# Optimization experiments

Hardware: AMD Instinct MI355X
Metric: run time of the kernel (lower is better)

The kernel has to match this reference:

```python
import jax, jax.numpy as jnp
import numpy as np

VOCAB, E, H, L, B, OUT = 50000, 300, 300, 75, 2048, 5

def setup_inputs() -> dict:
    key = jax.random.key(0)
    ks = jax.random.split(key, 12)
    s_e = 1.0 / np.sqrt(E)
    s_h = 1.0 / np.sqrt(H)
    return {
        "input_sequences": jax.random.randint(ks[0], (B, L), 0, VOCAB),
        "emb": jax.random.normal(ks[1], (VOCAB, E), jnp.float32) * 0.1,
        "W_ih": jax.random.normal(ks[2], (3 * H, E), jnp.float32) * s_e,
        "W_hh": jax.random.normal(ks[3], (3 * H, H), jnp.float32) * s_h,
        "b_ih": jax.random.normal(ks[4], (3 * H,), jnp.float32) * s_h,
        "b_hh": jax.random.normal(ks[5], (3 * H,), jnp.float32) * s_h,
        "wCo_w": jax.random.normal(ks[6], (3 * H,), jnp.float32) * (1.0 / np.sqrt(3 * H)),
        "wCo_b": jax.random.normal(ks[7], (1,), jnp.float32) * 0.02,
        "Wmy_w": jax.random.normal(ks[8], (L,), jnp.float32) * (1.0 / np.sqrt(L)),
        "Wmy_b": jax.random.normal(ks[9], (1,), jnp.float32) * 0.02,
        "logits_w": jax.random.normal(ks[10], (OUT, H), jnp.float32) * s_h,
        "logits_b": jax.random.normal(ks[11], (OUT,), jnp.float32) * 0.02,
    }

def _gru(x_tm, W_ih, W_hh, b_ih, b_hh):
    # x_tm: (L, B, E) time-major. PyTorch GRU cell math.
    gx_all = jnp.einsum("lbe,ge->lbg", x_tm, W_ih) + b_ih  # (L, B, 3H)
    h0 = jnp.zeros((x_tm.shape[1], W_hh.shape[1]), x_tm.dtype)
    def step(h, gx):
        gh = h @ W_hh.T + b_hh
        xr, xz, xn = jnp.split(gx, 3, axis=-1)
        hr, hz, hn = jnp.split(gh, 3, axis=-1)
        r = jax.nn.sigmoid(xr + hr)
        z = jax.nn.sigmoid(xz + hz)
        n = jnp.tanh(xn + r * hn)
        h_new = (1.0 - z) * n + z * h
        return h_new, h_new
    _, ys = jax.lax.scan(step, h0, gx_all)
    return ys  # (L, B, H)

def reference(input_sequences, emb, W_ih, W_hh, b_ih, b_hh,
              wCo_w, wCo_b, Wmy_w, Wmy_b, logits_w, logits_b):
    x = emb[input_sequences]                      # (B, L, E)
    out_tm = _gru(x.transpose(1, 0, 2), W_ih, W_hh, b_ih, b_hh)  # (L, B, H)
    h = out_tm.transpose(1, 0, 2)                 # (B, L, H)
    # co_attention: s_ij = wCo @ cat(h_i, h_j, h_i*h_j) + b
    # computed WITHOUT materializing the (B, L, L, 3H) tensor:
    wa, wb, wc = jnp.split(wCo_w, 3)
    a = h @ wa                                    # (B, L)
    b = h @ wb                                    # (B, L)
    c = jnp.einsum("bid,bjd->bij", h * wc, h)     # (B, L, L)
    s = a[:, :, None] + b[:, None, :] + c + wCo_b[0]
    # zero the diagonal (mask = ones - diag)
    s = s * (1.0 - jnp.eye(s.shape[1], dtype=s.dtype))
    # Wmy: Linear(75, 1) over the j axis
    sm = s @ Wmy_w + Wmy_b[0]                     # (B, L)
    attn = jax.nn.softmax(sm, axis=1)             # softmax over i
    pooled = jnp.einsum("bi,bih->bh", attn, h)    # (B, H)
    return pooled @ logits_w.T + logits_b         # (B, OUT)
```

## Files before the change

### kernel.cpp

```cpp
#include <hip/hip_runtime.h>
#include <stdint.h>


typedef float f32x4 __attribute__((ext_vector_type(4)));
typedef short bf16x8 __attribute__((ext_vector_type(8)));
typedef unsigned short u16;
typedef u16 u16x8 __attribute__((ext_vector_type(8)));
typedef u16 u16x4 __attribute__((ext_vector_type(4)));

#define DI __device__ __forceinline__

template <int N> struct IC { static constexpr int v = N; };

DI float bf2f(u16 v) {
    uint32_t u = ((uint32_t)v) << 16;
    float f;
    __builtin_memcpy(&f, &u, 4);
    return f;
}
DI u16 f2bf(float f) {
    uint32_t u;
    __builtin_memcpy(&u, &f, 4);
    uint32_t r = u + 0x7fffu + ((u >> 16) & 1u);
    return (u16)(r >> 16);
}
DI u16 cvt1(const void* p, int i, int f32m) {
    return f32m ? f2bf(((const float*)p)[i]) : ((const u16*)p)[i];
}

DI int hswz(int L, int kt) { return L ^ kt ^ (((L >> 4) & 3) << 1); }

DI u16x8 load_row8(const u16* __restrict__ base, int e0) {
    u16x4 z = {0, 0, 0, 0};
    u16x4 lo = (e0 < 300) ? *(const u16x4*)(base + e0) : z;
    u16x4 hi = (e0 + 4 < 300) ? *(const u16x4*)(base + e0 + 4) : z;
    u16x8 r;
    r[0] = lo[0]; r[1] = lo[1]; r[2] = lo[2]; r[3] = lo[3];
    r[4] = hi[0]; r[5] = hi[1]; r[6] = hi[2]; r[7] = hi[3];
    return r;
}
DI u16x8 load_row8_f32(const float* __restrict__ base, int e0) {
    f32x4 z = {0.f, 0.f, 0.f, 0.f};
    f32x4 lo = (e0 < 300) ? *(const f32x4*)(base + e0) : z;
    f32x4 hi = (e0 + 4 < 300) ? *(const f32x4*)(base + e0 + 4) : z;
    u16x8 r;
    r[0] = f2bf(lo[0]); r[1] = f2bf(lo[1]); r[2] = f2bf(lo[2]); r[3] = f2bf(lo[3]);
    r[4] = f2bf(hi[0]); r[5] = f2bf(hi[1]); r[6] = f2bf(hi[2]); r[7] = f2bf(hi[3]);
    return r;
}

__global__ __launch_bounds__(256) void detect_dtype(const u16* __restrict__ raw,
                                                    int* __restrict__ flag) {
    __shared__ int cnt;
    if (threadIdx.x == 0) cnt = 0;
    __syncthreads();
    int local = 0;
    for (int i = threadIdx.x; i < 4096; i += 256) {
        int e = (raw[i] >> 7) & 0xFF;
        if (e >= 140) local++;
    }
    atomicAdd(&cnt, local);
    __syncthreads();
    if (threadIdx.x == 0) flag[0] = (cnt > 256) ? 1 : 0;
}

__global__ __launch_bounds__(256) void conv_big(const void* __restrict__ in,
                                                u16* __restrict__ outp, int n,
                                                const int* __restrict__ flag) {
    const int f32m = flag[0];
    int i0 = (blockIdx.x * 256 + threadIdx.x) * 8;
#pragma unroll
    for (int k = 0; k < 8; k++) {
        int i = i0 + k;
        if (i < n) outp[i] = cvt1(in, i, f32m);
    }
}

__global__ __launch_bounds__(256) void conv_smalls(
    const void* bih_r, const void* bhh_r, const void* wCo_r, const void* wCob_r,
    const void* Wmy_r, const void* Wmyb_r, const void* lw_r, const void* lb_r,
    u16* __restrict__ smalls, const int* __restrict__ flag) {
    const int f32m = flag[0];
    int t = blockIdx.x * 256 + threadIdx.x;
    if (t < 900) smalls[t] = cvt1(bih_r, t, f32m);
    else if (t < 1800) smalls[1024 + t - 900] = cvt1(bhh_r, t - 900, f32m);
    else if (t < 2700) smalls[2048 + t - 1800] = cvt1(wCo_r, t - 1800, f32m);
    else if (t < 2775) smalls[3072 + t - 2700] = cvt1(Wmy_r, t - 2700, f32m);
    else if (t < 4275) smalls[3200 + t - 2775] = cvt1(lw_r, t - 2775, f32m);
    else if (t < 4280) smalls[4704 + t - 4275] = cvt1(lb_r, t - 4275, f32m);
    else if (t == 4280) smalls[4712] = cvt1(wCob_r, 0, f32m);
    else if (t == 4281) smalls[4713] = cvt1(Wmyb_r, 0, f32m);
}

__global__ __launch_bounds__(256) void prep_img(const u16* __restrict__ W,
                                                u16* __restrict__ img) {
    int t = blockIdx.x * 256 + threadIdx.x;
    if (t >= 60 * 10 * 64) return;
    int lane = t & 63;
    int kt = (t >> 6) % 10;
    int nt = t / 640;
    int g = nt * 16 + (lane & 15);
    int gate = g / 320, u = g - gate * 320;
    int e0 = kt * 32 + (lane >> 4) * 8;
    u16x8 v;
    if (u < 300) {
        v = load_row8(W + (size_t)(gate * 300 + u) * 300, e0);
    } else {
        u16x8 z = {0, 0, 0, 0, 0, 0, 0, 0};
        v = z;
    }
    *(u16x8*)&img[(size_t)t * 8] = v;
}

__global__ __launch_bounds__(256) void zero_hstate(float* __restrict__ hs) {
    int t = blockIdx.x * 256 + threadIdx.x;
    f32x4 z = {0.f, 0.f, 0.f, 0.f};
    ((f32x4*)hs)[t] = z;
}

__global__ __launch_bounds__(256, 2) void gemm1_kernel(
    const int* __restrict__ seq, const void* __restrict__ emb_raw,
    const u16* __restrict__ Wimg, const u16* __restrict__ bih,
    _Float16* __restrict__ gxn, int ck, int phase, int BC, int bshift,
    const int* __restrict__ flag) {
    __shared__ int ids[192];
    __shared__ __align__(16) u16 Aimg[12 * 64 * 8];
    __shared__ __align__(16) u16 Bbuf[12 * 64 * 8];

    const int tid = threadIdx.x;
    const int lane = tid & 63, wv = tid >> 6, q = lane >> 4, c = lane & 15;
    const int m0 = blockIdx.x * 192;
    const int nb = blockIdx.y;
    const int f32m = flag[0];
    const size_t PL = (size_t)15 * BC * 320;

    if (tid < 192) {
        int m = m0 + tid;
        int bc = m & (BC - 1);
        int tp = m >> bshift;
        ids[tid] = seq[(size_t)(phase * BC + bc) * 75 + ck * 15 + tp];
    }
    __syncthreads();

    f32x4 acc[3][12];
#pragma unroll
    for (int mt = 0; mt < 3; mt++)
#pragma unroll
        for (int nt = 0; nt < 12; nt++) {
            f32x4 z = {0.f, 0.f, 0.f, 0.f};
            acc[mt][nt] = z;
        }

    for (int kt = 0; kt < 10; kt++) {
#pragma unroll
        for (int s = 0; s < 3; s++) {
            int o = tid + s * 256;
            int qq = o / 192;
            int r = o - qq * 192;
            int e0 = kt * 32 + qq * 8;
            u16x8 v = f32m ? load_row8_f32((const float*)emb_raw + (size_t)ids[r] * 300, e0)
                           : load_row8((const u16*)emb_raw + (size_t)ids[r] * 300, e0);
            *(u16x8*)&Aimg[(((r >> 4) * 64) + ((r & 15) | (qq << 4))) * 8] = v;
        }
#pragma unroll
        for (int s = 0; s < 3; s++) {
            int ch = tid + s * 256;
            *(u16x8*)&Bbuf[ch * 8] =
                *(const u16x8*)&Wimg[(((size_t)(nb * 12 + (ch >> 6)) * 10 + kt) * 64 + (ch & 63)) * 8];
        }
        __syncthreads();

        bf16x8 a[3];
#pragma unroll
        for (int mt = 0; mt < 3; mt++) {
            u16x8 tmp = *(const u16x8*)&Aimg[(((wv * 3 + mt) * 64) + lane) * 8];
            a[mt] = __builtin_bit_cast(bf16x8, tmp);
        }
#pragma unroll
        for (int nt = 0; nt < 12; nt++) {
            u16x8 tb = *(const u16x8*)&Bbuf[(nt * 64 + lane) * 8];
            bf16x8 b = __builtin_bit_cast(bf16x8, tb);
#pragma unroll
            for (int mt = 0; mt < 3; mt++)
                acc[mt][nt] = __builtin_amdgcn_mfma_f32_16x16x32_bf16(a[mt], b, acc[mt][nt], 0, 0, 0);
        }
        __syncthreads();
    }

#pragma unroll
    for (int nt = 0; nt < 12; nt++) {
        int g = nb * 192 + nt * 16 + c;
        int gate = g / 320, u = g - gate * 320;
        float bias = (u < 300) ? bf2f(bih[gate * 300 + u]) : 0.f;
        _Float16* gp = gxn + (size_t)gate * PL;
#pragma unroll
        for (int mt = 0; mt < 3; mt++) {
            int mrow = m0 + (wv * 3 + mt) * 16 + q * 4;
#pragma unroll
            for (int reg = 0; reg < 4; reg++) {
                gp[(size_t)(mrow + reg) * 320 + u] = (_Float16)(acc[mt][nt][reg] + bias);
            }
        }
    }
}

__global__ __launch_bounds__(512, 1) void gru_chunk(
    const _Float16* __restrict__ gxn, const u16* __restrict__ Wimg,
    const u16* __restrict__ bhh_g, u16* __restrict__ h_all,
    float* __restrict__ hstate, int ck, int BC) {
    __shared__ __align__(16) u16 Hhi[10 * 64 * 8];
    __shared__ __align__(16) u16 Hlo[10 * 64 * 8];
    __shared__ __align__(16) u16 Wlds[61440];

    const int tid = threadIdx.x;
    const int lane = tid & 63, wv = tid >> 6, q = lane >> 4, c = lane & 15;
    const int b0 = blockIdx.x * 16;
    const int wbase = (wv < 4) ? wv * 9216 : 36864 + (wv - 4) * 6144;
    const size_t PL = (size_t)15 * BC * 320;

    float bhh[3][3];
    float hm[3][4];

    auto STAGE = [&](int kt, int buf, auto NTIC) {
        constexpr int NTI = NTIC.v;
        u16* dst = &Wlds[wbase + buf * (NTI * 3 * 512)];
#pragma unroll
        for (int Ti = 0; Ti < NTI; Ti++)
#pragma unroll
            for (int g = 0; g < 3; g++) {
                int nt = g * 20 + (wv + 8 * Ti);
                __builtin_amdgcn_global_load_lds(
                    (const unsigned int*)(Wimg + (size_t)(nt * 10 + kt) * 512 + lane * 8),
                    (unsigned int*)(dst + (Ti * 3 + g) * 512), 16, 0, 0);
            }
    };

    if (wv < 4) STAGE(0, 0, IC<3>{}); else STAGE(0, 0, IC<2>{});

    auto INIT = [&](auto NTIC) {
        constexpr int NTI = NTIC.v;
#pragma unroll
        for (int Ti = 0; Ti < NTI; Ti++) {
            int T = wv + 8 * Ti;
            int u = T * 16 + c;
#pragma unroll
            for (int g = 0; g < 3; g++)
                bhh[Ti][g] = (u < 300) ? bf2f(bhh_g[g * 300 + u]) : 0.f;
            int kti = T >> 1;
            int qp = ((T & 1) << 1) | (c >> 3);
            int j = c & 7;
#pragma unroll
            for (int reg = 0; reg < 4; reg++) {
                int m = q * 4 + reg;
                float h = hstate[(size_t)(b0 + m) * 320 + u];
                hm[Ti][reg] = h;
                int idx = (kti * 64 + ((q * 4 + reg) | (qp << 4))) * 8 + j;
                u16 hi = f2bf(h);
                Hhi[idx] = hi;
                Hlo[idx] = f2bf(h - bf2f(hi));
            }
        }
    };
    if (wv < 4) INIT(IC<3>{}); else INIT(IC<2>{});
    __syncthreads();

    for (int tt = 0; tt < 15; tt++) {
        auto PH1 = [&](auto NTIC) {
            constexpr int NTI = NTIC.v;
            constexpr int NT3 = NTI * 3;
            float gxr[NTI][4], gxz[NTI][4], gxnv[NTI][4];
#pragma unroll
            for (int Ti = 0; Ti < NTI; Ti++) {
                int u = (wv + 8 * Ti) * 16 + c;
#pragma unroll
                for (int reg = 0; reg < 4; reg++) {
                    int m = q * 4 + reg;
                    size_t idx = (size_t)((size_t)tt * BC + b0 + m) * 320 + u;
                    gxr[Ti][reg] = (float)gxn[idx];
                    gxz[Ti][reg] = (float)gxn[PL + idx];
                    gxnv[Ti][reg] = (float)gxn[2 * PL + idx];
                }
            }

            f32x4 acc[NTI][3];
#pragma unroll
            for (int Ti = 0; Ti < NTI; Ti++)
#pragma unroll
                for (int g = 0; g < 3; g++) {
                    f32x4 z = {0.f, 0.f, 0.f, 0.f};
                    acc[Ti][g] = z;
                }

#pragma unroll 2
            for (int kt = 0; kt < 10; kt++) {
                if (kt < 9) STAGE(kt + 1, (kt + 1) & 1, NTIC);
                else if (tt < 14) STAGE(0, 0, NTIC);
                if (kt == 9 && tt == 14) {
                    asm volatile("s_waitcnt vmcnt(0)" ::: "memory");
                } else if constexpr (NTI == 3) {
                    asm volatile("s_waitcnt vmcnt(9)" ::: "memory");
                } else {
                    asm volatile("s_waitcnt vmcnt(6)" ::: "memory");
                }

                u16x8 th = *(const u16x8*)&Hhi[(kt * 64 + lane) * 8];
                u16x8 tl = *(const u16x8*)&Hlo[(kt * 64 + lane) * 8];
                bf16x8 ahi = __builtin_bit_cast(bf16x8, th);
                bf16x8 alo = __builtin_bit_cast(bf16x8, tl);
                const u16* wb = &Wlds[wbase + (kt & 1) * (NT3 * 512)];
#pragma unroll
                for (int Ti = 0; Ti < NTI; Ti++)
#pragma unroll
                    for (int g = 0; g < 3; g++) {
                        u16x8 tb = *(const u16x8*)&wb[(Ti * 3 + g) * 512 + lane * 8];
                        bf16x8 b = __builtin_bit_cast(bf16x8, tb);
                        acc[Ti][g] = __builtin_amdgcn_mfma_f32_16x16x32_bf16(
                            ahi, b, acc[Ti][g], 0, 0, 0);
                        acc[Ti][g] = __builtin_amdgcn_mfma_f32_16x16x32_bf16(
                            alo, b, acc[Ti][g], 0, 0, 0);
                    }
            }

            const int tglob = ck * 15 + tt;
#pragma unroll
            for (int Ti = 0; Ti < NTI; Ti++) {
                int u = (wv + 8 * Ti) * 16 + c;
#pragma unroll
                for (int reg = 0; reg < 4; reg++) {
                    int m = q * 4 + reg;
                    float xr = gxr[Ti][reg];
                    float xz = gxz[Ti][reg];
                    float xn = gxnv[Ti][reg];
                    float hr = acc[Ti][0][reg] + bhh[Ti][0];
                    float hz = acc[Ti][1][reg] + bhh[Ti][1];
                    float hn = acc[Ti][2][reg] + bhh[Ti][2];
                    float r = 1.f / (1.f + __expf(-(xr + hr)));
                    float z = 1.f / (1.f + __expf(-(xz + hz)));
                    float ex = __expf(2.f * (xn + r * hn));
                    float n = 1.f - 2.f / (ex + 1.f);
                    float h = (1.f - z) * n + z * hm[Ti][reg];
                    hm[Ti][reg] = h;
                    h_all[((size_t)tglob * BC + (b0 + m)) * 320 + u] = f2bf(h);
                }
            }
        };
        if (wv < 4) PH1(IC<3>{}); else PH1(IC<2>{});
        __syncthreads();

        auto FRAG = [&](auto NTIC) {
            constexpr int NTI = NTIC.v;
#pragma unroll
            for (int Ti = 0; Ti < NTI; Ti++) {
                int T = wv + 8 * Ti;
                int kti = T >> 1;
                int qp = ((T & 1) << 1) | (c >> 3);
                int j = c & 7;
#pragma unroll
                for (int reg = 0; reg < 4; reg++) {
                    int idx = (kti * 64 + ((q * 4 + reg) | (qp << 4))) * 8 + j;
                    float h = hm[Ti][reg];
                    u16 hi = f2bf(h);
                    Hhi[idx] = hi;
                    Hlo[idx] = f2bf(h - bf2f(hi));
                }
            }
        };
        if (wv < 4) FRAG(IC<3>{}); else FRAG(IC<2>{});
        __syncthreads();
    }

    auto PERSIST = [&](auto NTIC) {
        constexpr int NTI = NTIC.v;
#pragma unroll
        for (int Ti = 0; Ti < NTI; Ti++) {
            int u = (wv + 8 * Ti) * 16 + c;
#pragma unroll
            for (int reg = 0; reg < 4; reg++) {
                int m = q * 4 + reg;
                hstate[(size_t)(b0 + m) * 320 + u] = hm[Ti][reg];
            }
        }
    };
    if (wv < 4) PERSIST(IC<3>{}); else PERSIST(IC<2>{});
}

__global__ __launch_bounds__(256) void coattn_kernel(
    const u16* __restrict__ h_all, const u16* __restrict__ smalls,
    void* __restrict__ outv, const int* __restrict__ flag, int phase, int BC) {
    __shared__ __align__(16) u16 himg[5 * 10 * 64 * 8];
    __shared__ float smacc[80], aArr[80], bArr[80], diagArr[80], attn[80], smv[80];
    __shared__ float scal[2];
    __shared__ float logitsAcc[5];

    const u16* wCo = smalls + 2048;
    const u16* Wmy = smalls + 3072;
    const u16* lw = smalls + 3200;
    const u16* lb = smalls + 4704;
    const int f32out = flag[0];

    const int b = blockIdx.x;
    const int tid = threadIdx.x;
    const int lane = tid & 63, wv = tid >> 6, q = lane >> 4, c = lane & 15;

    for (int o = tid; o < 3200; o += 256) {
        int i = o / 40;
        int oc = o - i * 40;
        int kt = oc >> 2, qq = oc & 3;
        int e0 = kt * 32 + qq * 8;
        u16x8 v = {0, 0, 0, 0, 0, 0, 0, 0};
        if (i < 75) v = *(const u16x8*)(h_all + ((size_t)i * BC + b) * 320 + e0);
        *(u16x8*)&himg[(((i >> 4) * 10 + kt) * 64 + hswz((i & 15) | (qq << 4), kt)) * 8] = v;
    }
    if (tid < 80) {
        smacc[tid] = 0.f; aArr[tid] = 0.f; bArr[tid] = 0.f;
        diagArr[tid] = 0.f; attn[tid] = 0.f;
    }
    if (tid < 5) logitsAcc[tid] = 0.f;
    __syncthreads();

    for (int pass = 0; pass < 2; pass++) {
        int nt = (pass == 0) ? wv : 4;
        int jj = nt * 16 + c;
        bf16x8 bfr[10];
#pragma unroll
        for (int kt = 0; kt < 10; kt++) {
            int e0 = kt * 32 + q * 8;
            u16x8 res = {0, 0, 0, 0, 0, 0, 0, 0};
            if (jj < 75) {
                u16x8 hv = *(const u16x8*)&himg[((nt * 10 + kt) * 64 + hswz(lane, kt)) * 8];
                u16x8 wcv = load_row8(wCo + 600, e0);
#pragma unroll
                for (int j = 0; j < 8; j++) res[j] = f2bf(bf2f(hv[j]) * bf2f(wcv[j]));
            } else if (jj == 75) {
                res = load_row8(wCo, e0);
            } else if (jj == 76) {
                res = load_row8(wCo + 300, e0);
            }
            bfr[kt] = __builtin_bit_cast(bf16x8, res);
        }
        float wmyj = (jj < 75) ? bf2f(Wmy[jj]) : 0.f;

        int nmt = (pass == 0) ? 5 : (wv == 0 ? 2 : 1);
        for (int mi = 0; mi < nmt; mi++) {
            int mt = (pass == 0) ? mi : (wv == 0 ? mi * 4 : wv);
            f32x4 acc = {0.f, 0.f, 0.f, 0.f};
#pragma unroll
            for (int kt = 0; kt < 10; kt++) {
                u16x8 ta = *(const u16x8*)&himg[((mt * 10 + kt) * 64 + hswz(lane, kt)) * 8];
                bf16x8 a = __builtin_bit_cast(bf16x8, ta);
                acc = __builtin_amdgcn_mfma_f32_16x16x32_bf16(a, bfr[kt], acc, 0, 0, 0);
            }
#pragma unroll
            for (int reg = 0; reg < 4; reg++) {
                int i = mt * 16 + q * 4 + reg;
                float v = acc[reg];
                float p = v * wmyj;
                p += __shfl_xor(p, 1);
                p += __shfl_xor(p, 2);
                p += __shfl_xor(p, 4);
                p += __shfl_xor(p, 8);
                if (c == 0 && i < 75) atomicAdd(&smacc[i], p);
                if (jj == i && i < 75) diagArr[i] = v;
                if (jj == 75) aArr[i] = v;
                if (jj == 76) bArr[i] = v;
            }
        }
    }
    __syncthreads();

    if (tid < 64) {
        float w1 = bf2f(Wmy[tid]);
        float w2 = (tid + 64 < 75) ? bf2f(Wmy[tid + 64]) : 0.f;
        float s1 = w1 + w2;
        float s2 = w1 * bArr[tid] + ((tid + 64 < 75) ? w2 * bArr[tid + 64] : 0.f);
#pragma unroll
        for (int m = 1; m < 64; m <<= 1) {
            s1 += __shfl_xor(s1, m);
            s2 += __shfl_xor(s2, m);
        }
        if (tid == 0) { scal[0] = s1; scal[1] = s2; }
    }
    __syncthreads();

    float cb = bf2f(smalls[4712]);
    float wmyb = bf2f(smalls[4713]);
    if (tid < 75) {
        float Wi = bf2f(Wmy[tid]);
        smv[tid] = smacc[tid] - diagArr[tid] * Wi + (aArr[tid] + cb) * (scal[0] - Wi) +
                   scal[1] - bArr[tid] * Wi + wmyb;
    }
    __syncthreads();

    if (tid < 64) {
        float v1 = smv[tid];
        float v2 = (tid + 64 < 75) ? smv[tid + 64] : -1e30f;
        float mx = fmaxf(v1, v2);
#pragma unroll
        for (int m = 1; m < 64; m <<= 1) mx = fmaxf(mx, __shfl_xor(mx, m));
        float e1 = __expf(v1 - mx);
        float e2 = (tid + 64 < 75) ? __expf(v2 - mx) : 0.f;
        float s = e1 + e2;
#pragma unroll
        for (int m = 1; m < 64; m <<= 1) s += __shfl_xor(s, m);
        attn[tid] = e1 / s;
        if (tid + 64 < 75) attn[tid + 64] = e2 / s;
    }
    __syncthreads();

    const int d1 = tid, d2 = tid + 256;
    float pd1 = 0.f, pd2 = 0.f;
    {
        const int kt1 = d1 >> 5, qq1 = (d1 >> 3) & 3, j1 = d1 & 7;
        const int kt2 = d2 >> 5, qq2 = (d2 >> 3) & 3, j2 = d2 & 7;
        for (int i = 0; i < 75; i++) {
            float a = attn[i];
            int ih = i >> 4, il = i & 15;
            pd1 += a * bf2f(himg[((ih * 10 + kt1) * 64 + hswz(il | (qq1 << 4), kt1)) * 8 + j1]);
            if (wv == 0)
                pd2 += a * bf2f(himg[((ih * 10 + kt2) * 64 + hswz(il | (qq2 << 4), kt2)) * 8 + j2]);
        }
    }
#pragma unroll
    for (int o = 0; o < 5; o++) {
        float part = (d1 < 300) ? pd1 * bf2f(lw[o * 300 + d1]) : 0.f;
        if (wv == 0 && d2 < 300) part += pd2 * bf2f(lw[o * 300 + d2]);
#pragma unroll
        for (int m = 1; m < 64; m <<= 1) part += __shfl_xor(part, m);
        if (lane == 0) atomicAdd(&logitsAcc[o], part);
    }
    __syncthreads();

    if (tid < 5) {
        float v = logitsAcc[tid] + bf2f(lb[tid]);
        size_t idx = (size_t)(phase * BC + b) * 5 + tid;
        if (f32out) ((float*)outv)[idx] = v;
        else ((u16*)outv)[idx] = f2bf(v);
    }
}

extern "C" void kernel_launch(void* const* d_in, const int* in_sizes, int n_in,
                              void* d_out, int out_size, void* d_ws, size_t ws_size,
                              hipStream_t stream) {
    const int* seq = (const int*)d_in[0];

    char* p = (char*)d_ws;
    int* flag = (int*)p;
    u16* smalls = (u16*)(p + 16);
    u16* WihImg = (u16*)(p + 9488);
    u16* WhhImg = (u16*)(p + 623888);
    u16* Wih_c = (u16*)(p + 1238288);
    u16* Whh_c = (u16*)(p + 1778288);
    const unsigned long long fixed_end = 2318288ull;

    auto req = [&](long long BC) -> unsigned long long {
        return fixed_end + (unsigned long long)BC * 87680ull + 1048576ull;
    };
    int BC = 256, bshift = 8;
    if (ws_size >= req(2048)) { BC = 2048; bshift = 11; }
    else if (ws_size >= req(1024)) { BC = 1024; bshift = 10; }
    else if (ws_size >= req(512)) { BC = 512; bshift = 9; }
    const int P = 2048 / BC;

    unsigned long long gx_b = 15ull * BC * 2560ull;
    unsigned long long h_b = 75ull * BC * 640ull;
    _Float16* gxn = (_Float16*)(p + fixed_end);
    u16* h_all = (u16*)(p + fixed_end + gx_b);
    float* hstate = (float*)(p + fixed_end + gx_b + h_b);

    detect_dtype<<<dim3(1), dim3(256), 0, stream>>>((const u16*)d_in[1], flag);
    conv_big<<<dim3((270000 + 2047) / 2048), dim3(256), 0, stream>>>(
        d_in[2], Wih_c, 270000, flag);
    conv_big<<<dim3((270000 + 2047) / 2048), dim3(256), 0, stream>>>(
        d_in[3], Whh_c, 270000, flag);
    conv_smalls<<<dim3(17), dim3(256), 0, stream>>>(
        d_in[4], d_in[5], d_in[6], d_in[7], d_in[8], d_in[9], d_in[10], d_in[11],
        smalls, flag);

    prep_img<<<dim3(150), dim3(256), 0, stream>>>(Wih_c, WihImg);
    prep_img<<<dim3(150), dim3(256), 0, stream>>>(Whh_c, WhhImg);

    for (int phase = 0; phase < P; phase++) {
        zero_hstate<<<dim3(BC * 320 / 1024), dim3(256), 0, stream>>>(hstate);
        for (int ck = 0; ck < 5; ck++) {
            gemm1_kernel<<<dim3(15 * BC / 192, 5), dim3(256), 0, stream>>>(
                seq, d_in[1], WihImg, smalls , gxn, ck, phase, BC, bshift, flag);
            gru_chunk<<<dim3(BC / 16), dim3(512), 0, stream>>>(
                gxn, WhhImg, smalls + 1024 , h_all, hstate, ck, BC);
        }
        coattn_kernel<<<dim3(BC), dim3(256), 0, stream>>>(h_all, smalls, d_out, flag,
                                                          phase, BC);
    }
}
```

Measured before the change: 1.280 ms.

## Use 10 waves per GRU block for a uniform two-tile split

The recurrent GRU kernel goes from 8 waves, which held an uneven 3/2 split of the 20 hidden-unit tiles, to 10 waves that each own exactly 2 tiles. Every wave now does the same work, so the per-step critical path is no longer set by the 3-tile waves, and the template-dispatch lambdas are removed. The first two weight k-tiles are now prefetched together at the start of each step, with adjusted waitcnt thresholds. The cost is more threads per block, with register pressure and barrier cost across 10 waves, and vmcnt counts that must stay exactly right for correctness.

Result: no change. 1.275 ms (-0.4%).

```diff
diff --git a/kernel.cpp b/kernel.cpp
--- a/kernel.cpp
+++ b/kernel.cpp
@@ -9,8 +9,6 @@
 typedef u16 u16x4 __attribute__((ext_vector_type(4)));
 
 #define DI __device__ __forceinline__
-
-template <int N> struct IC { static constexpr int v = N; };
 
 DI float bf2f(u16 v) {
     uint32_t u = ((uint32_t)v) << 16;
@@ -204,7 +202,7 @@
     }
 }
 
-__global__ __launch_bounds__(512, 1) void gru_chunk(
+__global__ __launch_bounds__(640, 1) void gru_chunk(
     const _Float16* __restrict__ gxn, const u16* __restrict__ Wimg,
     const u16* __restrict__ bhh_g, u16* __restrict__ h_all,
     float* __restrict__ hstate, int ck, int BC) {
@@ -215,173 +213,157 @@
     const int tid = threadIdx.x;
     const int lane = tid & 63, wv = tid >> 6, q = lane >> 4, c = lane & 15;
     const int b0 = blockIdx.x * 16;
-    const int wbase = (wv < 4) ? wv * 9216 : 36864 + (wv - 4) * 6144;
+    const int wbase = wv * 6144;
     const size_t PL = (size_t)15 * BC * 320;
 
-    float bhh[3][3];
-    float hm[3][4];
-
-    auto STAGE = [&](int kt, int buf, auto NTIC) {
-        constexpr int NTI = NTIC.v;
-        u16* dst = &Wlds[wbase + buf * (NTI * 3 * 512)];
-#pragma unroll
-        for (int Ti = 0; Ti < NTI; Ti++)
+    auto STAGE = [&](int kt, int buf) {
+        u16* dst = &Wlds[wbase + buf * 3072];
+#pragma unroll
+        for (int Ti = 0; Ti < 2; Ti++)
 #pragma unroll
             for (int g = 0; g < 3; g++) {
-                int nt = g * 20 + (wv + 8 * Ti);
+                int nt = g * 20 + (wv + 10 * Ti);
                 __builtin_amdgcn_global_load_lds(
                     (const unsigned int*)(Wimg + (size_t)(nt * 10 + kt) * 512 + lane * 8),
                     (unsigned int*)(dst + (Ti * 3 + g) * 512), 16, 0, 0);
             }
     };
 
-    if (wv < 4) STAGE(0, 0, IC<3>{}); else STAGE(0, 0, IC<2>{});
-
-    auto INIT = [&](auto NTIC) {
-        constexpr int NTI = NTIC.v;
-#pragma unroll
-        for (int Ti = 0; Ti < NTI; Ti++) {
-            int T = wv + 8 * Ti;
-            int u = T * 16 + c;
-#pragma unroll
-            for (int g = 0; g < 3; g++)
-                bhh[Ti][g] = (u < 300) ? bf2f(bhh_g[g * 300 + u]) : 0.f;
+    STAGE(0, 0);
+
+    float bhh[2][3];
+    float hm[2][4];
+#pragma unroll
+    for (int Ti = 0; Ti < 2; Ti++) {
+        int T = wv + 10 * Ti;
+        int u = T * 16 + c;
+#pragma unroll
+        for (int g = 0; g < 3; g++)
+            bhh[Ti][g] = (u < 300) ? bf2f(bhh_g[g * 300 + u]) : 0.f;
+        int kti = T >> 1;
+        int qp = ((T & 1) << 1) | (c >> 3);
+        int j = c & 7;
+#pragma unroll
+        for (int reg = 0; reg < 4; reg++) {
+            int m = q * 4 + reg;
+            float h = hstate[(size_t)(b0 + m) * 320 + u];
+            hm[Ti][reg] = h;
+            int idx = (kti * 64 + ((q * 4 + reg) | (qp << 4))) * 8 + j;
+            u16 hi = f2bf(h);
+            Hhi[idx] = hi;
+            Hlo[idx] = f2bf(h - bf2f(hi));
+        }
+    }
+    __syncthreads();
+
+    for (int tt = 0; tt < 15; tt++) {
+        STAGE(1, 1);
+
+        float gxr[2][4], gxz[2][4], gxnv[2][4];
+#pragma unroll
+        for (int Ti = 0; Ti < 2; Ti++) {
+            int u = (wv + 10 * Ti) * 16 + c;
+#pragma unroll
+            for (int reg = 0; reg < 4; reg++) {
+                int m = q * 4 + reg;
+                size_t idx = (size_t)((size_t)tt * BC + b0 + m) * 320 + u;
+                gxr[Ti][reg] = (float)gxn[idx];
+                gxz[Ti][reg] = (float)gxn[PL + idx];
+                gxnv[Ti][reg] = (float)gxn[2 * PL + idx];
+            }
+        }
+
+        f32x4 acc[2][3];
+#pragma unroll
+        for (int Ti = 0; Ti < 2; Ti++)
+#pragma unroll
+            for (int g = 0; g < 3; g++) {
+                f32x4 z = {0.f, 0.f, 0.f, 0.f};
+                acc[Ti][g] = z;
+            }
+
+#pragma unroll 2
+        for (int kt = 0; kt < 10; kt++) {
+            if (kt >= 1 && kt < 9) STAGE(kt + 1, (kt + 1) & 1);
+            else if (kt == 9 && tt < 14) STAGE(0, 0);
+
+            if (kt == 9 && tt == 14) {
+                asm volatile("s_waitcnt vmcnt(0)" ::: "memory");
+            } else if (kt < 2) {
+                asm volatile("s_waitcnt vmcnt(30)" ::: "memory");
+            } else {
+                asm volatile("s_waitcnt vmcnt(6)" ::: "memory");
+            }
+
+            u16x8 th = *(const u16x8*)&Hhi[(kt * 64 + lane) * 8];
+            u16x8 tl = *(const u16x8*)&Hlo[(kt * 64 + lane) * 8];
+            bf16x8 ahi = __builtin_bit_cast(bf16x8, th);
+            bf16x8 alo = __builtin_bit_cast(bf16x8, tl);
+            const u16* wb = &Wlds[wbase + (kt & 1) * 3072];
+#pragma unroll
+            for (int Ti = 0; Ti < 2; Ti++)
+#pragma unroll
+                for (int g = 0; g < 3; g++) {
+                    u16x8 tb = *(const u16x8*)&wb[(Ti * 3 + g) * 512 + lane * 8];
+                    bf16x8 b = __builtin_bit_cast(bf16x8, tb);
+                    acc[Ti][g] = __builtin_amdgcn_mfma_f32_16x16x32_bf16(
+                        ahi, b, acc[Ti][g], 0, 0, 0);
+                    acc[Ti][g] = __builtin_amdgcn_mfma_f32_16x16x32_bf16(
+                        alo, b, acc[Ti][g], 0, 0, 0);
+                }
+        }
+
+        const int tglob = ck * 15 + tt;
+#pragma unroll
+        for (int Ti = 0; Ti < 2; Ti++) {
+            int u = (wv + 10 * Ti) * 16 + c;
+#pragma unroll
+            for (int reg = 0; reg < 4; reg++) {
+                int m = q * 4 + reg;
+                float xr = gxr[Ti][reg];
+                float xz = gxz[Ti][reg];
+                float xn = gxnv[Ti][reg];
+                float hr = acc[Ti][0][reg] + bhh[Ti][0];
+                float hz = acc[Ti][1][reg] + bhh[Ti][1];
+                float hn = acc[Ti][2][reg] + bhh[Ti][2];
+                float r = 1.f / (1.f + __expf(-(xr + hr)));
+                float z = 1.f / (1.f + __expf(-(xz + hz)));
+                float ex = __expf(2.f * (xn + r * hn));
+                float n = 1.f - 2.f / (ex + 1.f);
+                float h = (1.f - z) * n + z * hm[Ti][reg];
+                hm[Ti][reg] = h;
+                h_all[((size_t)tglob * BC + (b0 + m)) * 320 + u] = f2bf(h);
+            }
+        }
+        __syncthreads();
+
+#pragma unroll
+        for (int Ti = 0; Ti < 2; Ti++) {
+            int T = wv + 10 * Ti;
             int kti = T >> 1;
             int qp = ((T & 1) << 1) | (c >> 3);
             int j = c & 7;
 #pragma unroll
             for (int reg = 0; reg < 4; reg++) {
-                int m = q * 4 + reg;
-                float h = hstate[(size_t)(b0 + m) * 320 + u];
-                hm[Ti][reg] = h;
                 int idx = (kti * 64 + ((q * 4 + reg) | (qp << 4))) * 8 + j;
+                float h = hm[Ti][reg];
                 u16 hi = f2bf(h);
                 Hhi[idx] = hi;
                 Hlo[idx] = f2bf(h - bf2f(hi));
             }
         }
-    };
-    if (wv < 4) INIT(IC<3>{}); else INIT(IC<2>{});
-    __syncthreads();
-
-    for (int tt = 0; tt < 15; tt++) {
-        auto PH1 = [&](auto NTIC) {
-            constexpr int NTI = NTIC.v;
-            constexpr int NT3 = NTI * 3;
-            float gxr[NTI][4], gxz[NTI][4], gxnv[NTI][4];
-#pragma unroll
-            for (int Ti = 0; Ti < NTI; Ti++) {
-                int u = (wv + 8 * Ti) * 16 + c;
-#pragma unroll
-                for (int reg = 0; reg < 4; reg++) {
-                    int m = q * 4 + reg;
-                    size_t idx = (size_t)((size_t)tt * BC + b0 + m) * 320 + u;
-                    gxr[Ti][reg] = (float)gxn[idx];
-                    gxz[Ti][reg] = (float)gxn[PL + idx];
-                    gxnv[Ti][reg] = (float)gxn[2 * PL + idx];
-                }
-            }
-
-            f32x4 acc[NTI][3];
-#pragma unroll
-            for (int Ti = 0; Ti < NTI; Ti++)
-#pragma unroll
-                for (int g = 0; g < 3; g++) {
-                    f32x4 z = {0.f, 0.f, 0.f, 0.f};
-                    acc[Ti][g] = z;
-                }
-
-#pragma unroll 2
-            for (int kt = 0; kt < 10; kt++) {
-                if (kt < 9) STAGE(kt + 1, (kt + 1) & 1, NTIC);
-                else if (tt < 14) STAGE(0, 0, NTIC);
-                if (kt == 9 && tt == 14) {
-                    asm volatile("s_waitcnt vmcnt(0)" ::: "memory");
-                } else if constexpr (NTI == 3) {
-                    asm volatile("s_waitcnt vmcnt(9)" ::: "memory");
-                } else {
-                    asm volatile("s_waitcnt vmcnt(6)" ::: "memory");
-                }
-
-                u16x8 th = *(const u16x8*)&Hhi[(kt * 64 + lane) * 8];
-                u16x8 tl = *(const u16x8*)&Hlo[(kt * 64 + lane) * 8];
-                bf16x8 ahi = __builtin_bit_cast(bf16x8, th);
-                bf16x8 alo = __builtin_bit_cast(bf16x8, tl);
-                const u16* wb = &Wlds[wbase + (kt & 1) * (NT3 * 512)];
-#pragma unroll
-                for (int Ti = 0; Ti < NTI; Ti++)
-#pragma unroll
-                    for (int g = 0; g < 3; g++) {
-                        u16x8 tb = *(const u16x8*)&wb[(Ti * 3 + g) * 512 + lane * 8];
-                        bf16x8 b = __builtin_bit_cast(bf16x8, tb);
-                        acc[Ti][g] = __builtin_amdgcn_mfma_f32_16x16x32_bf16(
-                            ahi, b, acc[Ti][g], 0, 0, 0);
-                        acc[Ti][g] = __builtin_amdgcn_mfma_f32_16x16x32_bf16(
-                            alo, b, acc[Ti][g], 0, 0, 0);
-                    }
-            }
-
-            const int tglob = ck * 15 + tt;
-#pragma unroll
-            for (int Ti = 0; Ti < NTI; Ti++) {
-                int u = (wv + 8 * Ti) * 16 + c;
-#pragma unroll
-                for (int reg = 0; reg < 4; reg++) {
-                    int m = q * 4 + reg;
-                    float xr = gxr[Ti][reg];
-                    float xz = gxz[Ti][reg];
-                    float xn = gxnv[Ti][reg];
-                    float hr = acc[Ti][0][reg] + bhh[Ti][0];
-                    float hz = acc[Ti][1][reg] + bhh[Ti][1];
-                    float hn = acc[Ti][2][reg] + bhh[Ti][2];
-                    float r = 1.f / (1.f + __expf(-(xr + hr)));
-                    float z = 1.f / (1.f + __expf(-(xz + hz)));
-                    float ex = __expf(2.f * (xn + r * hn));
-                    float n = 1.f - 2.f / (ex + 1.f);
-                    float h = (1.f - z) * n + z * hm[Ti][reg];
-                    hm[Ti][reg] = h;
-                    h_all[((size_t)tglob * BC + (b0 + m)) * 320 + u] = f2bf(h);
-                }
-            }
-        };
-        if (wv < 4) PH1(IC<3>{}); else PH1(IC<2>{});
         __syncthreads();
-
-        auto FRAG = [&](auto NTIC) {
-            constexpr int NTI = NTIC.v;
-#pragma unroll
-            for (int Ti = 0; Ti < NTI; Ti++) {
-                int T = wv + 8 * Ti;
-                int kti = T >> 1;
-                int qp = ((T & 1) << 1) | (c >> 3);
-                int j = c & 7;
-#pragma unroll
-                for (int reg = 0; reg < 4; reg++) {
-                    int idx = (kti * 64 + ((q * 4 + reg) | (qp << 4))) * 8 + j;
-                    float h = hm[Ti][reg];
-                    u16 hi = f2bf(h);
-                    Hhi[idx] = hi;
-                    Hlo[idx] = f2bf(h - bf2f(hi));
-                }
-            }
-        };
-        if (wv < 4) FRAG(IC<3>{}); else FRAG(IC<2>{});
-        __syncthreads();
-    }
-
-    auto PERSIST = [&](auto NTIC) {
-        constexpr int NTI = NTIC.v;
-#pragma unroll
-        for (int Ti = 0; Ti < NTI; Ti++) {
-            int u = (wv + 8 * Ti) * 16 + c;
-#pragma unroll
-            for (int reg = 0; reg < 4; reg++) {
-                int m = q * 4 + reg;
-                hstate[(size_t)(b0 + m) * 320 + u] = hm[Ti][reg];
-            }
-        }
-    };
-    if (wv < 4) PERSIST(IC<3>{}); else PERSIST(IC<2>{});
+    }
+
+#pragma unroll
+    for (int Ti = 0; Ti < 2; Ti++) {
+        int u = (wv + 10 * Ti) * 16 + c;
+#pragma unroll
+        for (int reg = 0; reg < 4; reg++) {
+            int m = q * 4 + reg;
+            hstate[(size_t)(b0 + m) * 320 + u] = hm[Ti][reg];
+        }
+    }
 }
 
 __global__ __launch_bounds__(256) void coattn_kernel(
@@ -584,7 +566,7 @@
         for (int ck = 0; ck < 5; ck++) {
             gemm1_kernel<<<dim3(15 * BC / 192, 5), dim3(256), 0, stream>>>(
                 seq, d_in[1], WihImg, smalls , gxn, ck, phase, BC, bshift, flag);
-            gru_chunk<<<dim3(BC / 16), dim3(512), 0, stream>>>(
+            gru_chunk<<<dim3(BC / 16), dim3(640), 0, stream>>>(
                 gxn, WhhImg, smalls + 1024 , h_all, hstate, ck, BC);
         }
         coattn_kernel<<<dim3(BC), dim3(256), 0, stream>>>(h_all, smalls, d_out, flag,
```
